# Performance work log

Measured on AMD Instinct MI355X. Metric: run time of the kernel, lower is better.

The kernel has to match this reference:

```python
import jax, jax.numpy as jnp
import numpy as np

B, C, H, W = 4, 32, 64, 64
K = 3
HEADS = 8
SF = 4
D = C * K * K          # 288, unfold token dim
E = D // 2             # 144, reduced dim
DH = E // HEADS        # 18, head dim
SCALE = DH ** -0.5
N = H * W              # 4096 tokens


def unfold(x):
    # x: (B,C,H,W) -> (B, C*K*K, H*W), torch.nn.Unfold ordering (c, kh, kw)
    xp = jnp.pad(x, ((0, 0), (0, 0), (1, 1), (1, 1)))
    patches = jnp.stack([xp[:, :, i:i + H, j:j + W] for i in range(K) for j in range(K)], axis=2)
    return patches.reshape(x.shape[0], C * K * K, H * W)


def fold(cols):
    # inverse of unfold: scatter-add overlapping patches back, crop padding
    b = cols.shape[0]
    y = cols.reshape(b, C, K, K, H, W)
    out = jnp.zeros((b, C, H + 2, W + 2), cols.dtype)
    for i in range(K):
        for j in range(K):
            out = out.at[:, :, i:i + H, j:j + W].add(y[:, :, i, j])
    return out[:, :, 1:-1, 1:-1]


def layernorm_cols(cols, g, b):
    # LayerNorm over D applied on (B,N,D) view, returned as (B,D,N)
    xt = cols.transpose(0, 2, 1)
    mu = xt.mean(-1, keepdims=True)
    var = xt.var(-1, keepdims=True)
    y = (xt - mu) / jnp.sqrt(var + 1e-5) * g + b
    return y.transpose(0, 2, 1)


def emha(x, wr, br, wqkv, we, be):
    # x: (B, D, N)
    b, _, n_tok = x.shape
    xr = jnp.einsum('bdn,ed->ben', x, wr) + br[None, :, None]   # Conv1d k=1 reduction
    t = xr.transpose(0, 2, 1)                                   # (B,N,E)
    qkv = t @ wqkv.T                                            # Linear, no bias
    q, k, v = jnp.split(qkv, 3, axis=-1)
    n = n_tok // SF

    def rs(a):
        return a.reshape(b, n_tok, HEADS, DH).transpose(0, 2, 1, 3).reshape(b, HEADS, SF, n, DH)

    q, k, v = rs(q), rs(k), rs(v)
    attn = jax.nn.softmax(jnp.einsum('bhsnd,bhsmd->bhsnm', q, k) * SCALE, axis=-1)
    o = jnp.einsum('bhsnm,bhsmd->bhsnd', attn, v)
    o = o.reshape(b, HEADS, n_tok, DH).transpose(0, 2, 1, 3).reshape(b, n_tok, E).transpose(0, 2, 1)
    return jnp.einsum('ben,fe->bfn', o, we) + be[None, :, None]  # Conv1d k=1 expansion


def conv3x3(x, w, b):
    y = jax.lax.conv_general_dilated(x, w, (1, 1), ((1, 1), (1, 1)),
                                     dimension_numbers=('NCHW', 'OIHW', 'NCHW'))
    return y + b[None, :, None, None]


def setup_inputs() -> dict:
    key = jax.random.key(0)
    ks = jax.random.split(key, 20)
    s = 0.02
    inp = {
        'x': jax.random.normal(ks[0], (B, C, H, W), jnp.float32),
        'ln_g': jnp.ones((D,), jnp.float32),
        'ln_b': jnp.zeros((D,), jnp.float32),
        'conv_w': jax.random.normal(ks[1], (C, C, 3, 3), jnp.float32) * s,
        'conv_b': jnp.zeros((C,), jnp.float32),
    }
    for i in range(3):
        k0, k1, k2 = jax.random.split(ks[2 + i], 3)
        inp[f'wr{i+1}'] = jax.random.normal(k0, (E, D), jnp.float32) * s
        inp[f'br{i+1}'] = jnp.zeros((E,), jnp.float32)
        inp[f'wqkv{i+1}'] = jax.random.normal(k1, (3 * E, E), jnp.float32) * s
        inp[f'we{i+1}'] = jax.random.normal(k2, (D, E), jnp.float32) * s
        inp[f'be{i+1}'] = jnp.zeros((D,), jnp.float32)
    return inp


def reference(x, ln_g, ln_b, conv_w, conv_b,
              wr1, br1, wqkv1, we1, be1,
              wr2, br2, wqkv2, we2, be2,
              wr3, br3, wqkv3, we3, be3):
    t = x
    for (wr, br, wqkv, we, be) in ((wr1, br1, wqkv1, we1, be1),
                                   (wr2, br2, wqkv2, we2, be2),
                                   (wr3, br3, wqkv3, we3, be3)):
        cols = unfold(t)
        cols_n = layernorm_cols(cols, ln_g, ln_b)
        cols = emha(cols_n, wr, br, wqkv, we, be) + cols
        t = fold(cols)
    return x + jax.nn.elu(conv3x3(t, conv_w, conv_b))
```

## Files before the change

### kernel.cpp

```cpp
#include <hip/hip_runtime.h>
#include <math.h>

#define BN 4
#define CC 32
#define HH 64
#define WW 64
#define DD 288
#define EE 144
#define NTOK 4096
#define SCALE_F 0.2357022603955158f
#define QSCALE  0.3401074286f
#define QST 192
#define KST 32
#define MQKV 528

typedef __bf16 bf16x8 __attribute__((ext_vector_type(8)));
typedef float floatx4 __attribute__((ext_vector_type(4)));
typedef unsigned short u16x8 __attribute__((ext_vector_type(8)));
typedef short s16x4 __attribute__((ext_vector_type(4)));

__device__ __forceinline__ unsigned short f2bf(float x) {
    unsigned int u = __float_as_uint(x);
    u += 0x7fffu + ((u >> 16) & 1u);
    return (unsigned short)(u >> 16);
}
__device__ __forceinline__ float bf2f(unsigned short s) {
    return __uint_as_float(((unsigned int)s) << 16);
}
__device__ __forceinline__ unsigned int pack_bf_trunc(float a, float b) {
    return __builtin_amdgcn_perm(__float_as_uint(b), __float_as_uint(a), 0x07060302u);
}

__global__ __launch_bounds__(256) void setup_k(
    const float* __restrict__ wr0, const float* __restrict__ br0,
    const float* __restrict__ wr1, const float* __restrict__ br1,
    const float* __restrict__ wr2, const float* __restrict__ br2,
    const float* __restrict__ g,  const float* __restrict__ lb,
    const float* __restrict__ wqkv0, const float* __restrict__ wqkv1, const float* __restrict__ wqkv2,
    const float* __restrict__ we0,   const float* __restrict__ we1,   const float* __restrict__ we2,
    unsigned short* __restrict__ wg_bf, float* __restrict__ wgsum, float* __restrict__ wbeta,
    unsigned short* __restrict__ wqkv_bf, unsigned short* __restrict__ we_bf)
{
    int blk = blockIdx.x;
    int tid = threadIdx.x;
    if (blk < 3) {
        if (tid < 144) {
            int l = blk, e = tid;
            const float* wr = (l == 0) ? wr0 : ((l == 1) ? wr1 : wr2);
            const float* br = (l == 0) ? br0 : ((l == 1) ? br1 : br2);
            float sg = 0.f, sb = 0.f;
            for (int d = 0; d < DD; ++d) {
                float w = wr[e * DD + d];
                float wgv = w * g[d];
                wg_bf[((size_t)l * EE + e) * DD + d] = f2bf(wgv);
                sg += wgv;
                sb += w * lb[d];
            }
            wgsum[l * EE + e] = sg;
            wbeta[l * EE + e] = sb + br[e];
        }
        return;
    }
    int idx = (blk - 3) * 256 + tid;
    const int T1 = 3 * MQKV * 160;
    const int T2 = 3 * 288 * 160;
    if (idx < T1) {
        int l = idx / (MQKV * 160), r = idx % (MQKV * 160);
        int m = r / 160, k = r % 160;
        const float* w = (l == 0) ? wqkv0 : ((l == 1) ? wqkv1 : wqkv2);
        float v = 0.f;
        if (k < 144) {
            if (m < 192) {
                int h = m / 24, j = m % 24;
                if (j < 18) v = w[(h * 18 + j) * 144 + k] * QSCALE;
            } else if (m < 384) {
                int mm = m - 192, h = mm / 24, j = mm % 24;
                if (j < 18) v = w[(144 + h * 18 + j) * 144 + k];
            } else {
                v = w[(288 + (m - 384)) * 144 + k];
            }
        }
        wqkv_bf[idx] = f2bf(v);
    } else if (idx < T1 + T2) {
        int j = idx - T1;
        int l = j / (288 * 160), r = j % (288 * 160);
        int m = r / 160, k = r % 160;
        const float* w = (l == 0) ? we0 : ((l == 1) ? we1 : we2);
        we_bf[j] = (k < 144) ? f2bf(w[m * 144 + k]) : 0;
    }
}

__global__ __launch_bounds__(512) void fgemm1_k(
    const float* __restrict__ t, const unsigned short* __restrict__ wg,
    const float* __restrict__ wgsum, const float* __restrict__ wbeta,
    unsigned short* __restrict__ xrT)
{
    __shared__ unsigned short Cs[64 * 296];
    __shared__ float red1[8][64], red2[8][64];
    int tid = threadIdx.x;
    int lane = tid & 63, part = tid >> 6;
    int b = blockIdx.x >> 6, nc = blockIdx.x & 63;
    int w = lane;
    const float* tb = t + (size_t)b * CC * HH * WW;
    __attribute__((aligned(8))) unsigned short loc[36];
    float s1 = 0.f, s2 = 0.f;
    #pragma unroll
    for (int c4 = 0; c4 < 4; ++c4) {
        int c = part * 4 + c4;
        const float* tc = tb + (size_t)c * 4096;
        #pragma unroll
        for (int i = 0; i < 3; ++i) {
            int hr = nc + i - 1;
            bool rok = ((unsigned)hr < 64u);
            #pragma unroll
            for (int j = 0; j < 3; ++j) {
                int wc = w + j - 1;
                bool ok = rok && ((unsigned)wc < 64u);
                float v = ok ? tc[hr * 64 + wc] : 0.f;
                loc[c4 * 9 + i * 3 + j] = f2bf(v);
                s1 += v;
                s2 = fmaf(v, v, s2);
            }
        }
    }
    {
        unsigned short* cr = &Cs[lane * 296 + part * 36];
        #pragma unroll
        for (int k = 0; k < 9; ++k)
            *(unsigned long long*)&cr[k * 4] = *(const unsigned long long*)&loc[k * 4];
    }
    red1[part][lane] = s1;
    red2[part][lane] = s2;
    __syncthreads();
    if (tid < 64) {
        float a = 0.f, q = 0.f;
        #pragma unroll
        for (int p = 0; p < 8; ++p) { a += red1[p][tid]; q += red2[p][tid]; }
        float m = a * (1.f / 288.f);
        float var = q * (1.f / 288.f) - m * m;
        red1[0][tid] = m;
        red2[0][tid] = rsqrtf(var + 1e-5f);
    }
    __syncthreads();

    int l15 = lane & 15, l4 = lane >> 4;
    int tw = part & 3, mh = part >> 2;
    const unsigned short* Ar = wg + (size_t)(mh * 16 + l15) * DD + l4 * 8;
    floatx4 acc[5];
    #pragma unroll
    for (int i = 0; i < 5; ++i) acc[i] = (floatx4){0.f, 0.f, 0.f, 0.f};
    #pragma unroll
    for (int ks = 0; ks < 9; ++ks) {
        bf16x8 bfr = *(const bf16x8*)&Cs[(tw * 16 + l15) * 296 + ks * 32 + l4 * 8];
        #pragma unroll
        for (int i = 0; i < 4; ++i) {
            bf16x8 af = *(const bf16x8*)(Ar + (size_t)i * 32 * DD + ks * 32);
            acc[i] = __builtin_amdgcn_mfma_f32_16x16x32_bf16(af, bfr, acc[i], 0, 0, 0);
        }
        if (mh == 0) {
            bf16x8 af = *(const bf16x8*)(Ar + (size_t)4 * 32 * DD + ks * 32);
            acc[4] = __builtin_amdgcn_mfma_f32_16x16x32_bf16(af, bfr, acc[4], 0, 0, 0);
        }
    }

    __syncthreads();
    {
        int tok = tw * 16 + l15;
        float muv = red1[0][tok], rsv = red2[0][tok];
        #pragma unroll
        for (int i = 0; i < 5; ++i) {
            if (i == 4 && mh) break;
            #pragma unroll
            for (int r = 0; r < 4; ++r) {
                int m = (mh + 2 * i) * 16 + l4 * 4 + r;
                float v = rsv * (acc[i][r] - muv * wgsum[m]) + wbeta[m];
                Cs[tok * 296 + m] = f2bf(v);
            }
        }
    }
    __syncthreads();
    for (int u = tid; u < 64 * 20; u += 512) {
        int row = u / 20, seg = u - row * 20;
        unsigned short* dst = xrT + ((size_t)b * NTOK + nc * 64 + row) * 160 + seg * 8;
        u16x8 val = (seg < 18) ? *(const u16x8*)&Cs[row * 296 + seg * 8] : (u16x8)0;
        *(u16x8*)dst = val;
    }
}

template<int K, int MODE, int NYB>
__global__ __launch_bounds__(256) void mgemm_k(
    const unsigned short* __restrict__ A, const unsigned short* __restrict__ Bt, int BST,
    unsigned short* __restrict__ Ct, unsigned short* __restrict__ Cv, unsigned short* __restrict__ Ck,
    const float* __restrict__ bias)
{
    constexpr int NT = 64;
    __shared__ unsigned short Ts[64 * 56];
    int flat = blockIdx.x;
    int g  = (flat / (8 * NYB)) * 8 + (flat & 7);
    int jm = (flat % (8 * NYB)) >> 3;
    int n0 = (g & 63) * NT;
    int bI = g >> 6;
    int m0 = jm * 48;
    int tid = threadIdx.x;
    int wv = tid >> 6, lane = tid & 63;
    int l15 = lane & 15, l4 = lane >> 4;

    const unsigned short* Arow = A + (size_t)(m0 + l15) * K + l4 * 8;
    const unsigned short* Brow = Bt + ((size_t)bI * NTOK + n0 + wv * 16 + l15) * BST + l4 * 8;

    floatx4 acc[3];
    acc[0] = acc[1] = acc[2] = (floatx4){0.f, 0.f, 0.f, 0.f};

    #pragma unroll
    for (int ks = 0; ks < K / 32; ++ks) {
        bf16x8 bfr = *(const bf16x8*)(Brow + ks * 32);
        #pragma unroll
        for (int mi = 0; mi < 3; ++mi) {
            bf16x8 af = *(const bf16x8*)(Arow + (size_t)mi * 16 * K + ks * 32);
            acc[mi] = __builtin_amdgcn_mfma_f32_16x16x32_bf16(af, bfr, acc[mi], 0, 0, 0);
        }
    }

    int n_l = wv * 16 + l15;

    if (MODE == 2) {
        #pragma unroll
        for (int mi = 0; mi < 3; ++mi)
            #pragma unroll
            for (int r = 0; r < 4; ++r) {
                int m_l = mi * 16 + l4 * 4 + r;
                Ts[m_l * 72 + n_l] = f2bf(acc[mi][r] + bias[m0 + m_l]);
            }
        __syncthreads();
        for (int u = tid; u < 48 * 8; u += 256) {
            int row = u >> 3, seg = u & 7;
            unsigned short* dst = Ct + ((size_t)bI * DD + m0 + row) * NTOK + n0 + seg * 8;
            *(u16x8*)dst = *(const u16x8*)&Ts[row * 72 + seg * 8];
        }
    } else {
        bool vpath = (m0 >= 384);
        #pragma unroll
        for (int mi = 0; mi < 3; ++mi)
            #pragma unroll
            for (int r = 0; r < 4; ++r) {
                int m_l = mi * 16 + l4 * 4 + r;
                float v = acc[mi][r];
                if (!vpath) Ts[n_l * 56 + m_l] = f2bf(v);
                else        Ts[m_l * 72 + n_l] = f2bf(v);
            }
        __syncthreads();
        if (!vpath) {
            if (tid < 128) {
                int row = tid >> 1, half = tid & 1;
                const unsigned short* src = &Ts[row * 56 + half * 24];
                if (m0 >= 192) {
                    int head = (m0 - 192) / 24 + half;
                    unsigned short* dst = Ck + ((size_t)(bI * 8 + head) * NTOK + n0 + row) * KST;
                    #pragma unroll
                    for (int u = 0; u < 3; ++u)
                        *(u16x8*)&dst[u * 8] = *(const u16x8*)&src[u * 8];
                    *(u16x8*)&dst[24] = (u16x8)0;
                } else {
                    unsigned short* dst = Ct + ((size_t)bI * NTOK + n0 + row) * QST + m0 + half * 24;
                    #pragma unroll
                    for (int u = 0; u < 3; ++u)
                        *(u16x8*)&dst[u * 8] = *(const u16x8*)&src[u * 8];
                }
            }
        } else {
            for (int u = tid; u < 48 * 8; u += 256) {
                int row = u >> 3, seg = u & 7;
                unsigned short* dst = Cv + ((size_t)bI * EE + (m0 - 384) + row) * NTOK + n0 + seg * 8;
                *(u16x8*)dst = *(const u16x8*)&Ts[row * 72 + seg * 8];
            }
        }
    }
}

__global__ __launch_bounds__(256, 4) void attn_k2(const unsigned short* __restrict__ qT,
                                                  const unsigned short* __restrict__ kP,
                                                  const unsigned short* __restrict__ vF,
                                                  unsigned short* __restrict__ oT)
{
    __shared__ unsigned short Vs[32 * 136];

    int blk = blockIdx.x;
    int bhs = blk & 127;
    int qc  = blk >> 7;
    int b = bhs >> 5, h = (bhs >> 2) & 7, s = bhs & 3;
    int tid  = threadIdx.x;
    int wv   = tid >> 6;
    int lane = tid & 63;
    int l15 = lane & 15, l4 = lane >> 4;
    int q0 = qc * 64;
    int tokbase = s * 1024;

    for (int v = tid; v < 14 * 16; v += 256) {
        int d = 18 + (v >> 4), seg = v & 15;
        unsigned short val = (d == 31) ? (unsigned short)0x3F80 : (unsigned short)0;
        u16x8 vv = (u16x8)val;
        *(u16x8*)&Vs[d * 136 + seg * 8] = vv;
    }

    bf16x8 qf;
    {
        u16x8 raw = *(const u16x8*)(qT + ((size_t)b * NTOK + tokbase + q0 + wv * 16 + l15) * QST
                                    + 24 * h + l4 * 8);
        if (l4 == 3) raw = (u16x8)0;
        qf = *(bf16x8*)&raw;
    }

    floatx4 oacc[2];
    oacc[0] = (floatx4){0.f, 0.f, 0.f, 0.f};
    oacc[1] = (floatx4){0.f, 0.f, 0.f, 0.f};

    const unsigned short* vbb = vF + (size_t)b * EE * NTOK + tokbase;
    int d0 = tid >> 4, seg0 = tid & 15;
    bool x2 = (tid < 32);
    int d1 = 16 + (tid >> 4), seg1 = tid & 15;
    u16x8 pv0, pv1;
    pv0 = *(const u16x8*)(vbb + (size_t)(h * 18 + d0) * NTOK + seg0 * 8);
    if (x2) pv1 = *(const u16x8*)(vbb + (size_t)(h * 18 + d1) * NTOK + seg1 * 8);

    const unsigned short* kRow = kP + ((size_t)(b * 8 + h) * NTOK + tokbase + l15) * KST + l4 * 8;

    for (int c0 = 0; c0 < 1024; c0 += 128) {
        bf16x8 kreg[8];
        #pragma unroll
        for (int sub = 0; sub < 2; ++sub)
            #pragma unroll
            for (int mi = 0; mi < 4; ++mi) {
                u16x8 raw = *(const u16x8*)(kRow + (unsigned)(c0 + sub * 64 + mi * 16) * KST);
                kreg[sub * 4 + mi] = *(bf16x8*)&raw;
            }

        __syncthreads();
        *(u16x8*)&Vs[d0 * 136 + seg0 * 8] = pv0;
        if (x2) *(u16x8*)&Vs[d1 * 136 + seg1 * 8] = pv1;
        int cn = c0 + 128;
        if (cn < 1024) {
            pv0 = *(const u16x8*)(vbb + (size_t)(h * 18 + d0) * NTOK + cn + seg0 * 8);
            if (x2) pv1 = *(const u16x8*)(vbb + (size_t)(h * 18 + d1) * NTOK + cn + seg1 * 8);
        }
        __syncthreads();

        #pragma unroll
        for (int sub = 0; sub < 2; ++sub) {
            floatx4 sacc[4];
            #pragma unroll
            for (int mi = 0; mi < 4; ++mi) {
                floatx4 z = (floatx4){0.f, 0.f, 0.f, 0.f};
                sacc[mi] = __builtin_amdgcn_mfma_f32_16x16x32_bf16(kreg[sub * 4 + mi], qf, z, 0, 0, 0);
            }

            unsigned int pk0[4], pk1[4];
            #pragma unroll
            for (int mi = 0; mi < 4; ++mi) {
                pk0[mi] = pack_bf_trunc(exp2f(sacc[mi][0]), exp2f(sacc[mi][1]));
                pk1[mi] = pack_bf_trunc(exp2f(sacc[mi][2]), exp2f(sacc[mi][3]));
            }

            #pragma unroll
            for (int tt = 0; tt < 4; ++tt) {
                union { unsigned int u[2]; s16x4 v; } pb;
                pb.u[0] = pk0[tt]; pb.u[1] = pk1[tt];
                #pragma unroll
                for (int nd = 0; nd < 2; ++nd) {
                    s16x4 af = *(const s16x4*)&Vs[(nd * 16 + l15) * 136 + sub * 64 + tt * 16 + l4 * 4];
                    oacc[nd] = __builtin_amdgcn_mfma_f32_16x16x16bf16_1k(af, pb.v, oacc[nd], 0, 0, 0);
                }
            }
        }
    }

    float lsum = __shfl(oacc[1][3], 48 + l15, 64);
    float inv  = 1.f / lsum;
    size_t rowi = (size_t)b * NTOK + tokbase + q0 + wv * 16 + l15;
    unsigned short* orow = oT + rowi * 160 + h * 18;
    unsigned int w0 = (unsigned)f2bf(oacc[0][0] * inv) | ((unsigned)f2bf(oacc[0][1] * inv) << 16);
    unsigned int w1 = (unsigned)f2bf(oacc[0][2] * inv) | ((unsigned)f2bf(oacc[0][3] * inv) << 16);
    *(unsigned int*)&orow[l4 * 4]     = w0;
    *(unsigned int*)&orow[l4 * 4 + 2] = w1;
    if (l4 == 0) {
        unsigned int w2 = (unsigned)f2bf(oacc[1][0] * inv) | ((unsigned)f2bf(oacc[1][1] * inv) << 16);
        *(unsigned int*)&orow[16] = w2;
    }
    if (h == 7 && l4 < 2) {
        u16x8 z = (u16x8)0;
        *(u16x8*)(oT + rowi * 160 + 144 + l4 * 8) = z;
    }
}

__global__ __launch_bounds__(256) void fold_k(const unsigned short* __restrict__ cols,
                                              const float* __restrict__ tprev,
                                              float* __restrict__ t)
{
    int idx = blockIdx.x * 256 + threadIdx.x;
    int w = idx & 63;
    int h = (idx >> 6) & 63;
    int c = (idx >> 12) & 31;
    int b = idx >> 17;
    const unsigned short* cb = cols + (size_t)b * DD * NTOK + (size_t)c * 9 * NTOK;
    float sum = 0.f;
    #pragma unroll
    for (int i = 0; i < 3; ++i) {
        int hs = h + 1 - i;
        if ((unsigned)hs < 64u) {
            #pragma unroll
            for (int j = 0; j < 3; ++j) {
                int ws_ = w + 1 - j;
                if ((unsigned)ws_ < 64u)
                    sum += bf2f(cb[(size_t)(i * 3 + j) * NTOK + hs * 64 + ws_]);
            }
        }
    }
    int ch = (h == 0 || h == 63) ? 2 : 3;
    int cw_ = (w == 0 || w == 63) ? 2 : 3;
    t[idx] = sum + (float)(ch * cw_) * tprev[idx];
}

__global__ __launch_bounds__(256) void conv_k(const float* __restrict__ t,
    const float* __restrict__ cw, const float* __restrict__ cbias,
    const float* __restrict__ x, float* __restrict__ out)
{
    __shared__ float wsh[CC * 9];
    int blk = blockIdx.x;
    int band = blk & 3, co = (blk >> 2) & 31, b = blk >> 7;
    int tid = threadIdx.x;
    for (int u = tid; u < CC * 9; u += 256) wsh[u] = cw[co * CC * 9 + u];
    __syncthreads();
    int h = band * 16 + (tid >> 4);
    int w0 = (tid & 15) << 2;
    const float* tb = t + (size_t)b * CC * 4096;
    float bias = cbias[co];
    float a0 = bias, a1 = bias, a2 = bias, a3 = bias;
    for (int ci = 0; ci < CC; ++ci) {
        const float* tc = tb + (size_t)ci * 4096;
        const float* wr = &wsh[ci * 9];
        #pragma unroll
        for (int i = 0; i < 3; ++i) {
            int hr = h + i - 1;
            if ((unsigned)hr < 64u) {
                const float* row = tc + hr * 64;
                float vl = (w0 > 0)  ? row[w0 - 1] : 0.f;
                float4 c4 = *(const float4*)&row[w0];
                float vr = (w0 < 60) ? row[w0 + 4] : 0.f;
                float wj0 = wr[i * 3], wj1 = wr[i * 3 + 1], wj2 = wr[i * 3 + 2];
                a0 = fmaf(wj0, vl,   a0); a0 = fmaf(wj1, c4.x, a0); a0 = fmaf(wj2, c4.y, a0);
                a1 = fmaf(wj0, c4.x, a1); a1 = fmaf(wj1, c4.y, a1); a1 = fmaf(wj2, c4.z, a1);
                a2 = fmaf(wj0, c4.y, a2); a2 = fmaf(wj1, c4.z, a2); a2 = fmaf(wj2, c4.w, a2);
                a3 = fmaf(wj0, c4.z, a3); a3 = fmaf(wj1, c4.w, a3); a3 = fmaf(wj2, vr,   a3);
            }
        }
    }
    size_t oidx = ((size_t)(b * CC + co) * 4096) + h * 64 + w0;
    float4 xin = *(const float4*)&x[oidx];
    float4 o;
    o.x = xin.x + ((a0 > 0.f) ? a0 : (__expf(a0) - 1.f));
    o.y = xin.y + ((a1 > 0.f) ? a1 : (__expf(a1) - 1.f));
    o.z = xin.z + ((a2 > 0.f) ? a2 : (__expf(a2) - 1.f));
    o.w = xin.w + ((a3 > 0.f) ? a3 : (__expf(a3) - 1.f));
    *(float4*)&out[oidx] = o;
}

extern "C" void kernel_launch(void* const* d_in, const int* in_sizes, int n_in,
                              void* d_out, int out_size, void* d_ws, size_t ws_size,
                              hipStream_t stream)
{
    const float* x    = (const float*)d_in[0];
    const float* ln_g = (const float*)d_in[1];
    const float* ln_b = (const float*)d_in[2];
    const float* cw   = (const float*)d_in[3];
    const float* cb   = (const float*)d_in[4];
    const float* wr[3]   = {(const float*)d_in[5],  (const float*)d_in[10], (const float*)d_in[15]};
    const float* br[3]   = {(const float*)d_in[6],  (const float*)d_in[11], (const float*)d_in[16]};
    const float* wqkv[3] = {(const float*)d_in[7],  (const float*)d_in[12], (const float*)d_in[17]};
    const float* we[3]   = {(const float*)d_in[8],  (const float*)d_in[13], (const float*)d_in[18]};
    const float* be[3]   = {(const float*)d_in[9],  (const float*)d_in[14], (const float*)d_in[19]};
    float* out = (float*)d_out;

    char* p = (char*)d_ws;
    unsigned short* cols_bf = (unsigned short*)p; p += (size_t)BN * DD * NTOK * 2;
    unsigned short* oT    = (unsigned short*)p; p += (size_t)BN * NTOK * 288 * 2;
    unsigned short* xrT   = (unsigned short*)p; p += (size_t)BN * NTOK * 160 * 2;
    unsigned short* qT    = (unsigned short*)p; p += (size_t)BN * NTOK * QST * 2;
    unsigned short* kP    = (unsigned short*)p; p += (size_t)BN * 8 * NTOK * KST * 2;
    unsigned short* vF    = (unsigned short*)p; p += (size_t)BN * EE * NTOK * 2;
    float* tA   = (float*)p;              p += (size_t)BN * CC * HH * WW * 4;
    float* tB   = (float*)p;              p += (size_t)BN * CC * HH * WW * 4;
    unsigned short* wg_bf   = (unsigned short*)p; p += (size_t)3 * EE * DD * 2;
    unsigned short* wqkv_bf = (unsigned short*)p; p += (size_t)3 * MQKV * 160 * 2;
    unsigned short* we_bf   = (unsigned short*)p; p += (size_t)3 * DD * 160 * 2;
    float* wgsum = (float*)p;             p += 3 * EE * 4;
    float* wbeta = (float*)p;             p += 3 * EE * 4;
    (void)in_sizes; (void)n_in; (void)out_size; (void)ws_size;

    setup_k<<<1533, 256, 0, stream>>>(wr[0], br[0], wr[1], br[1], wr[2], br[2], ln_g, ln_b,
                                      wqkv[0], wqkv[1], wqkv[2], we[0], we[1], we[2],
                                      wg_bf, wgsum, wbeta, wqkv_bf, we_bf);

    const float* tin = x;
    float* touts[3] = {tA, tB, tA};
    for (int l = 0; l < 3; ++l) {
        fgemm1_k<<<256, 512, 0, stream>>>(tin, wg_bf + (size_t)l * EE * DD,
                                          wgsum + l * EE, wbeta + l * EE, xrT);
        mgemm_k<160, 0, 11><<<2816, 256, 0, stream>>>(
            wqkv_bf + (size_t)l * MQKV * 160, xrT, 160, qT, vF, kP, nullptr);
        attn_k2<<<2048, 256, 0, stream>>>(qT, kP, vF, oT);
        mgemm_k<160, 2, 6><<<1536, 256, 0, stream>>>(
            we_bf + (size_t)l * DD * 160, oT, 160, cols_bf, nullptr, nullptr, be[l]);
        fold_k<<<2048, 256, 0, stream>>>(cols_bf, tin, touts[l]);
        tin = touts[l];
    }
    conv_k<<<512, 256, 0, stream>>>(tA, cw, cb, x, out);
}
```

Baseline: 420.7 us.

## Restructure attention kernel: register V fragments, permlane P reshuffle, two query tiles per wave

```diff
diff --git a/kernel.cpp b/kernel.cpp
--- a/kernel.cpp
+++ b/kernel.cpp
@@ -17,7 +17,6 @@
 typedef __bf16 bf16x8 __attribute__((ext_vector_type(8)));
 typedef float floatx4 __attribute__((ext_vector_type(4)));
 typedef unsigned short u16x8 __attribute__((ext_vector_type(8)));
-typedef short s16x4 __attribute__((ext_vector_type(4)));
 
 __device__ __forceinline__ unsigned short f2bf(float x) {
     unsigned int u = __float_as_uint(x);
@@ -29,6 +28,12 @@
 }
 __device__ __forceinline__ unsigned int pack_bf_trunc(float a, float b) {
     return __builtin_amdgcn_perm(__float_as_uint(b), __float_as_uint(a), 0x07060302u);
+}
+__device__ __forceinline__ void plswap32(unsigned int& a, unsigned int& b) {
+    asm("v_permlane32_swap_b32 %0, %1" : "+v"(a), "+v"(b));
+}
+__device__ __forceinline__ void plswap16(unsigned int& a, unsigned int& b) {
+    asm("v_permlane16_swap_b32 %0, %1" : "+v"(a), "+v"(b));
 }
 
 __global__ __launch_bounds__(256) void setup_k(
@@ -282,8 +287,6 @@
                                                   const unsigned short* __restrict__ vF,
                                                   unsigned short* __restrict__ oT)
 {
-    __shared__ unsigned short Vs[32 * 136];
-
     int blk = blockIdx.x;
     int bhs = blk & 127;
     int qc  = blk >> 7;
@@ -292,102 +295,103 @@
     int wv   = tid >> 6;
     int lane = tid & 63;
     int l15 = lane & 15, l4 = lane >> 4;
-    int q0 = qc * 64;
+    int q0 = qc * 128;
     int tokbase = s * 1024;
 
-    for (int v = tid; v < 14 * 16; v += 256) {
-        int d = 18 + (v >> 4), seg = v & 15;
-        unsigned short val = (d == 31) ? (unsigned short)0x3F80 : (unsigned short)0;
-        u16x8 vv = (u16x8)val;
-        *(u16x8*)&Vs[d * 136 + seg * 8] = vv;
-    }
-
-    bf16x8 qf;
-    {
-        u16x8 raw = *(const u16x8*)(qT + ((size_t)b * NTOK + tokbase + q0 + wv * 16 + l15) * QST
+    bf16x8 qf[2];
+    #pragma unroll
+    for (int ni = 0; ni < 2; ++ni) {
+        u16x8 raw = *(const u16x8*)(qT + ((size_t)b * NTOK + tokbase + q0 + wv * 32 + ni * 16 + l15) * QST
                                     + 24 * h + l4 * 8);
         if (l4 == 3) raw = (u16x8)0;
-        qf = *(bf16x8*)&raw;
-    }
-
-    floatx4 oacc[2];
-    oacc[0] = (floatx4){0.f, 0.f, 0.f, 0.f};
-    oacc[1] = (floatx4){0.f, 0.f, 0.f, 0.f};
-
-    const unsigned short* vbb = vF + (size_t)b * EE * NTOK + tokbase;
-    int d0 = tid >> 4, seg0 = tid & 15;
-    bool x2 = (tid < 32);
-    int d1 = 16 + (tid >> 4), seg1 = tid & 15;
-    u16x8 pv0, pv1;
-    pv0 = *(const u16x8*)(vbb + (size_t)(h * 18 + d0) * NTOK + seg0 * 8);
-    if (x2) pv1 = *(const u16x8*)(vbb + (size_t)(h * 18 + d1) * NTOK + seg1 * 8);
+        qf[ni] = *(bf16x8*)&raw;
+    }
+
+    floatx4 oacc[2][2];
+    #pragma unroll
+    for (int ni = 0; ni < 2; ++ni)
+        #pragma unroll
+        for (int nd = 0; nd < 2; ++nd)
+            oacc[ni][nd] = (floatx4){0.f, 0.f, 0.f, 0.f};
+    float psum[2] = {0.f, 0.f};
 
     const unsigned short* kRow = kP + ((size_t)(b * 8 + h) * NTOK + tokbase + l15) * KST + l4 * 8;
+    const unsigned short* vRow = vF + ((size_t)b * EE + h * 18) * NTOK + tokbase;
 
     for (int c0 = 0; c0 < 1024; c0 += 128) {
-        bf16x8 kreg[8];
-        #pragma unroll
-        for (int sub = 0; sub < 2; ++sub)
-            #pragma unroll
-            for (int mi = 0; mi < 4; ++mi) {
-                u16x8 raw = *(const u16x8*)(kRow + (unsigned)(c0 + sub * 64 + mi * 16) * KST);
-                kreg[sub * 4 + mi] = *(bf16x8*)&raw;
-            }
-
-        __syncthreads();
-        *(u16x8*)&Vs[d0 * 136 + seg0 * 8] = pv0;
-        if (x2) *(u16x8*)&Vs[d1 * 136 + seg1 * 8] = pv1;
-        int cn = c0 + 128;
-        if (cn < 1024) {
-            pv0 = *(const u16x8*)(vbb + (size_t)(h * 18 + d0) * NTOK + cn + seg0 * 8);
-            if (x2) pv1 = *(const u16x8*)(vbb + (size_t)(h * 18 + d1) * NTOK + cn + seg1 * 8);
-        }
-        __syncthreads();
-
         #pragma unroll
         for (int sub = 0; sub < 2; ++sub) {
-            floatx4 sacc[4];
-            #pragma unroll
-            for (int mi = 0; mi < 4; ++mi) {
-                floatx4 z = (floatx4){0.f, 0.f, 0.f, 0.f};
-                sacc[mi] = __builtin_amdgcn_mfma_f32_16x16x32_bf16(kreg[sub * 4 + mi], qf, z, 0, 0, 0);
-            }
-
-            unsigned int pk0[4], pk1[4];
-            #pragma unroll
-            for (int mi = 0; mi < 4; ++mi) {
-                pk0[mi] = pack_bf_trunc(exp2f(sacc[mi][0]), exp2f(sacc[mi][1]));
-                pk1[mi] = pack_bf_trunc(exp2f(sacc[mi][2]), exp2f(sacc[mi][3]));
-            }
-
-            #pragma unroll
-            for (int tt = 0; tt < 4; ++tt) {
-                union { unsigned int u[2]; s16x4 v; } pb;
-                pb.u[0] = pk0[tt]; pb.u[1] = pk1[tt];
+            int base = c0 + sub * 64;
+            bf16x8 vfr[2][2];
+            #pragma unroll
+            for (int c = 0; c < 2; ++c)
                 #pragma unroll
                 for (int nd = 0; nd < 2; ++nd) {
-                    s16x4 af = *(const s16x4*)&Vs[(nd * 16 + l15) * 136 + sub * 64 + tt * 16 + l4 * 4];
-                    oacc[nd] = __builtin_amdgcn_mfma_f32_16x16x16bf16_1k(af, pb.v, oacc[nd], 0, 0, 0);
+                    u16x8 raw = *(const u16x8*)(vRow + (size_t)(nd * 16 + l15) * NTOK
+                                                + base + c * 32 + l4 * 8);
+                    vfr[c][nd] = *(bf16x8*)&raw;
                 }
-            }
-        }
-    }
-
-    float lsum = __shfl(oacc[1][3], 48 + l15, 64);
-    float inv  = 1.f / lsum;
-    size_t rowi = (size_t)b * NTOK + tokbase + q0 + wv * 16 + l15;
-    unsigned short* orow = oT + rowi * 160 + h * 18;
-    unsigned int w0 = (unsigned)f2bf(oacc[0][0] * inv) | ((unsigned)f2bf(oacc[0][1] * inv) << 16);
-    unsigned int w1 = (unsigned)f2bf(oacc[0][2] * inv) | ((unsigned)f2bf(oacc[0][3] * inv) << 16);
-    *(unsigned int*)&orow[l4 * 4]     = w0;
-    *(unsigned int*)&orow[l4 * 4 + 2] = w1;
-    if (l4 == 0) {
-        unsigned int w2 = (unsigned)f2bf(oacc[1][0] * inv) | ((unsigned)f2bf(oacc[1][1] * inv) << 16);
-        *(unsigned int*)&orow[16] = w2;
-    }
-    if (h == 7 && l4 < 2) {
-        u16x8 z = (u16x8)0;
-        *(u16x8*)(oT + rowi * 160 + 144 + l4 * 8) = z;
+            bf16x8 kf[4];
+            #pragma unroll
+            for (int mi = 0; mi < 4; ++mi) {
+                u16x8 raw = *(const u16x8*)(kRow + (unsigned)(base + mi * 16) * KST);
+                kf[mi] = *(bf16x8*)&raw;
+            }
+
+            #pragma unroll
+            for (int ni = 0; ni < 2; ++ni) {
+                floatx4 sacc[4];
+                #pragma unroll
+                for (int mi = 0; mi < 4; ++mi) {
+                    floatx4 z = (floatx4){0.f, 0.f, 0.f, 0.f};
+                    sacc[mi] = __builtin_amdgcn_mfma_f32_16x16x32_bf16(kf[mi], qf[ni], z, 0, 0, 0);
+                }
+                unsigned int pk0[4], pk1[4];
+                #pragma unroll
+                for (int mi = 0; mi < 4; ++mi) {
+                    float e0 = exp2f(sacc[mi][0]), e1 = exp2f(sacc[mi][1]);
+                    float e2 = exp2f(sacc[mi][2]), e3 = exp2f(sacc[mi][3]);
+                    psum[ni] += (e0 + e1) + (e2 + e3);
+                    pk0[mi] = pack_bf_trunc(e0, e1);
+                    pk1[mi] = pack_bf_trunc(e2, e3);
+                }
+                #pragma unroll
+                for (int c = 0; c < 2; ++c) {
+                    unsigned int B0 = pk0[2 * c], B2 = pk0[2 * c + 1];
+                    unsigned int B1 = pk1[2 * c], B3 = pk1[2 * c + 1];
+                    plswap32(B0, B2); plswap16(B0, B2);
+                    plswap32(B1, B3); plswap16(B1, B3);
+                    union { unsigned int u[4]; bf16x8 v; } bfr;
+                    bfr.u[0] = B0; bfr.u[1] = B1; bfr.u[2] = B2; bfr.u[3] = B3;
+                    #pragma unroll
+                    for (int nd = 0; nd < 2; ++nd)
+                        oacc[ni][nd] = __builtin_amdgcn_mfma_f32_16x16x32_bf16(vfr[c][nd], bfr.v,
+                                                                               oacc[ni][nd], 0, 0, 0);
+                }
+            }
+        }
+    }
+
+    #pragma unroll
+    for (int ni = 0; ni < 2; ++ni) {
+        float p = psum[ni];
+        p += __shfl_xor(p, 16, 64);
+        p += __shfl_xor(p, 32, 64);
+        float inv = 1.f / p;
+        size_t rowi = (size_t)b * NTOK + tokbase + q0 + wv * 32 + ni * 16 + l15;
+        unsigned short* orow = oT + rowi * 160 + h * 18;
+        unsigned int w0 = (unsigned)f2bf(oacc[ni][0][0] * inv) | ((unsigned)f2bf(oacc[ni][0][1] * inv) << 16);
+        unsigned int w1 = (unsigned)f2bf(oacc[ni][0][2] * inv) | ((unsigned)f2bf(oacc[ni][0][3] * inv) << 16);
+        *(unsigned int*)&orow[l4 * 4]     = w0;
+        *(unsigned int*)&orow[l4 * 4 + 2] = w1;
+        if (l4 == 0) {
+            unsigned int w2 = (unsigned)f2bf(oacc[ni][1][0] * inv) | ((unsigned)f2bf(oacc[ni][1][1] * inv) << 16);
+            *(unsigned int*)&orow[16] = w2;
+        }
+        if (h == 7 && l4 < 2) {
+            u16x8 z = (u16x8)0;
+            *(u16x8*)(oT + rowi * 160 + 144 + l4 * 8) = z;
+        }
     }
 }
 
@@ -506,7 +510,7 @@
                                           wgsum + l * EE, wbeta + l * EE, xrT);
         mgemm_k<160, 0, 11><<<2816, 256, 0, stream>>>(
             wqkv_bf + (size_t)l * MQKV * 160, xrT, 160, qT, vF, kP, nullptr);
-        attn_k2<<<2048, 256, 0, stream>>>(qT, kP, vF, oT);
+        attn_k2<<<1024, 256, 0, stream>>>(qT, kP, vF, oT);
         mgemm_k<160, 2, 6><<<1536, 256, 0, stream>>>(
             we_bf + (size_t)l * DD * 160, oT, 160, cols_bf, nullptr, nullptr, be[l]);
         fold_k<<<2048, 256, 0, stream>>>(cols_bf, tin, touts[l]);
```

After: 452.7 us. 1.08x slower.
